# Performance work log

Measured on AMD Instinct MI355X. Metric: run time of the kernel, lower is better.

## Reference

```python
import jax, jax.numpy as jnp
import numpy as np

C = 256
DK = C // 8  # query/key channels


def setup_inputs() -> dict:
    key = jax.random.key(0)
    ks = jax.random.split(key, 7)
    B, W, H = 4, 64, 64
    x = jax.random.normal(ks[0], (B, C, W, H), dtype=jnp.float32)
    s_in = 1.0 / np.sqrt(C)
    Wq = jax.random.normal(ks[1], (DK, C), dtype=jnp.float32) * s_in
    bq = jnp.zeros((DK,), dtype=jnp.float32)
    Wk = jax.random.normal(ks[2], (DK, C), dtype=jnp.float32) * s_in
    bk = jnp.zeros((DK,), dtype=jnp.float32)
    Wv = jax.random.normal(ks[3], (C, C), dtype=jnp.float32) * s_in
    bv = jnp.zeros((C,), dtype=jnp.float32)
    return {"x": x, "Wq": Wq, "bq": bq, "Wk": Wk, "bk": bk, "Wv": Wv, "bv": bv}


def reference(x, Wq, bq, Wk, bk, Wv, bv):
    B, Cc, W, H = x.shape
    N = W * H
    xf = x.reshape(B, Cc, N)  # (B, C, N) flattened spatial
    # 1x1 convs == channel matmuls
    q = jnp.einsum('dc,bcn->bnd', Wq, xf) + bq  # (B, N, DK)
    k = jnp.einsum('dc,bcn->bdn', Wk, xf) + bk[None, :, None]  # (B, DK, N)
    v = jnp.einsum('oc,bcn->bon', Wv, xf) + bv[None, :, None]  # (B, C, N)
    energy = jnp.einsum('bnd,bdm->bnm', q, k) / jnp.sqrt(jnp.float32(q.shape[-1]))
    attn = jax.nn.softmax(energy, axis=-1)  # (B, N, N)
    out = jnp.einsum('bcn,bmn->bcm', v, attn)  # v @ attn^T
    return out.reshape(B, Cc, W, H) + x
```

## Files before the change

kernel.cpp:

```cpp
#include <hip/hip_runtime.h>
#include <hip/hip_bf16.h>
#include <math.h>

#define BB 4
#define CC 256
#define DKK 32
#define NN 4096
#define QSCALE2 0.25503489022324213f

typedef __attribute__((ext_vector_type(8))) __bf16 bf16x8;
typedef __attribute__((ext_vector_type(4))) __bf16 bf16x4;
typedef __attribute__((ext_vector_type(4))) float f32x4;

#define XROW 264

__global__ __launch_bounds__(256) void qkv2_kernel(
    const float* __restrict__ x,
    const float* __restrict__ Wq, const float* __restrict__ Wk,
    const float* __restrict__ Wv,
    const float* __restrict__ bq, const float* __restrict__ bk,
    const float* __restrict__ bv,
    __bf16* __restrict__ qws, __bf16* __restrict__ kws, __bf16* __restrict__ vws)
{
    __shared__ __align__(16) unsigned char smemB[32 * XROW * 2];
    __bf16* xs = (__bf16*)smemB;
    float (*scr)[33] = (float (*)[33])smemB;

    const int tid = threadIdx.x;
    const int w   = tid >> 6;
    const int l   = tid & 63;
    const int l15 = l & 15;
    const int lq  = l >> 4;
    const int n0  = blockIdx.x * 32;
    const int b   = blockIdx.y;

    {
        const int cl = tid >> 3;
        const int nf = (tid & 7) * 4;
#pragma unroll
        for (int p = 0; p < 8; p++) {
            int c = p * 32 + cl;
            float4 v = *(const float4*)&x[((size_t)(b * CC + c)) * NN + n0 + nf];
            xs[(nf + 0) * XROW + c] = (__bf16)v.x;
            xs[(nf + 1) * XROW + c] = (__bf16)v.y;
            xs[(nf + 2) * XROW + c] = (__bf16)v.z;
            xs[(nf + 3) * XROW + c] = (__bf16)v.w;
        }
    }

    const float* wrow[5];
#pragma unroll
    for (int ot = 0; ot < 5; ot++) {
        int ob = 80 * w + ot * 16;
        const float* mat; int r0;
        if (ob < 32)      { mat = Wq; r0 = ob; }
        else if (ob < 64) { mat = Wk; r0 = ob - 32; }
        else              { mat = Wv; r0 = ob - 64; }
        wrow[ot] = mat + (size_t)(r0 + l15) * CC + lq * 8;
    }

    __syncthreads();

    const f32x4 zf = {0.f, 0.f, 0.f, 0.f};
    f32x4 acc[5][2];
#pragma unroll
    for (int i = 0; i < 5; i++)
#pragma unroll
        for (int j = 0; j < 2; j++) acc[i][j] = zf;

    const __bf16* xls = &xs[l15 * XROW + lq * 8];

    bf16x8 bcur[2], acur[5], bnxt[2], anxt[5];
#pragma unroll
    for (int nt = 0; nt < 2; nt++) bcur[nt] = *(const bf16x8*)(xls + nt * 16 * XROW);
#pragma unroll
    for (int ot = 0; ot < 5; ot++) {
        f32x4 a0 = *(const f32x4*)(wrow[ot]);
        f32x4 a1 = *(const f32x4*)(wrow[ot] + 4);
        bf16x8 af;
#pragma unroll
        for (int j = 0; j < 4; j++) { af[j] = (__bf16)a0[j]; af[4 + j] = (__bf16)a1[j]; }
        acur[ot] = af;
    }

#pragma unroll
    for (int ks = 0; ks < 8; ks++) {
        if (ks < 7) {
#pragma unroll
            for (int nt = 0; nt < 2; nt++)
                bnxt[nt] = *(const bf16x8*)(xls + nt * 16 * XROW + (ks + 1) * 32);
#pragma unroll
            for (int ot = 0; ot < 5; ot++) {
                f32x4 a0 = *(const f32x4*)(wrow[ot] + (ks + 1) * 32);
                f32x4 a1 = *(const f32x4*)(wrow[ot] + (ks + 1) * 32 + 4);
                bf16x8 af;
#pragma unroll
                for (int j = 0; j < 4; j++) { af[j] = (__bf16)a0[j]; af[4 + j] = (__bf16)a1[j]; }
                anxt[ot] = af;
            }
        }
#pragma unroll
        for (int ot = 0; ot < 5; ot++)
#pragma unroll
            for (int nt = 0; nt < 2; nt++)
                acc[ot][nt] = __builtin_amdgcn_mfma_f32_16x16x32_bf16(acur[ot], bcur[nt], acc[ot][nt], 0, 0, 0);
        if (ks < 7) {
#pragma unroll
            for (int nt = 0; nt < 2; nt++) bcur[nt] = bnxt[nt];
#pragma unroll
            for (int ot = 0; ot < 5; ot++) acur[ot] = anxt[ot];
        }
    }

    __syncthreads();

    __bf16* vchunk = vws + (size_t)b * CC * NN + (size_t)(n0 >> 5) * 16 * 512;
#pragma unroll
    for (int ot = 0; ot < 5; ot++) {
        int ob = 80 * w + ot * 16;
#pragma unroll
        for (int nt = 0; nt < 2; nt++) {
#pragma unroll
            for (int r = 0; r < 4; r++) {
                int o = ob + lq * 4 + r;
                int n = nt * 16 + l15;
                float val = acc[ot][nt][r];
                if (ob >= 64) {
                    int c = o - 64;
                    vchunk[(5 * w - 4 + ot) * 512 + (lq * 4 + r) * 32 + n] =
                        (__bf16)(val + bv[c]);
                } else if (ob < 32) {
                    scr[o][n] = (val + bq[o]) * QSCALE2;
                } else {
                    scr[o][n] = val + bk[o - 32];
                }
            }
        }
    }
    __syncthreads();
    {
        int n  = tid >> 3;
        int d0 = (tid & 7) * 4;
        bf16x4 qv, kv;
#pragma unroll
        for (int j = 0; j < 4; j++) {
            qv[j] = (__bf16)scr[d0 + j][n];
            kv[j] = (__bf16)scr[32 + d0 + j][n];
        }
        size_t base = ((size_t)b * NN + n0 + n) * DKK + d0;
        *(bf16x4*)&qws[base] = qv;
        *(bf16x4*)&kws[base] = kv;
    }
}

#define PST 40
#define MST 68
#define PWSZ (64 * PST)

__global__ __launch_bounds__(256, 2) void attn_kernel(
    const __bf16* __restrict__ qb, const __bf16* __restrict__ kb,
    const __bf16* __restrict__ vt, const float* __restrict__ x,
    float* __restrict__ out)
{
    __shared__ __align__(16) unsigned char smem[42240];
    __bf16* pw   = (__bf16*)smem + (threadIdx.x >> 6) * 2 * PWSZ;
    float*  Ls   = (float*)(smem + 40960);
    float*  Linv = (float*)(smem + 41984);

    const int tid = threadIdx.x;
    const int w   = tid >> 6;
    const int l   = tid & 63;
    const int l15 = l & 15;
    const int lq  = l >> 4;

    const int beta = blockIdx.x;
    const int b    = (beta >> 1) & 3;
    const int ch   = (beta >> 3) & 1;
    const int mt   = ((beta >> 4) << 1) | (beta & 1);
    const int m0   = mt * 64;

    const __bf16* qbb = qb + (size_t)b * NN * DKK;
    const __bf16* kbb = kb + (size_t)b * NN * DKK;
    const __bf16* vtb = vt + (size_t)b * CC * NN;

    bf16x8 qa[4];
#pragma unroll
    for (int af = 0; af < 4; af++)
        qa[af] = *(const bf16x8*)(qbb + (size_t)(m0 + af * 16 + l15) * DKK + lq * 8);

    const __bf16* kstrip = kbb + (size_t)(w * 32 + l15) * DKK + lq * 8;
    const __bf16* vstrip = vtb + (size_t)w * 8192 + (size_t)ch * 4096
                               + l15 * 32 + lq * 8;

    const f32x4 zf = {0.f, 0.f, 0.f, 0.f};
    f32x4 acc[4][8];
#pragma unroll
    for (int i = 0; i < 4; i++)
#pragma unroll
        for (int j = 0; j < 8; j++) acc[i][j] = zf;
    float lacc[4] = {0.f, 0.f, 0.f, 0.f};

    bf16x8 kA0 = *(const bf16x8*)kstrip;
    bf16x8 kA1 = *(const bf16x8*)(kstrip + 16 * DKK);
#pragma unroll
    for (int af = 0; af < 4; af++) {
        f32x4 e0 = __builtin_amdgcn_mfma_f32_16x16x32_bf16(kA0, qa[af], zf, 0, 0, 0);
        f32x4 e1 = __builtin_amdgcn_mfma_f32_16x16x32_bf16(kA1, qa[af], zf, 0, 0, 0);
        bf16x4 p0, p1;
#pragma unroll
        for (int r = 0; r < 4; r++) {
            float v0 = __builtin_amdgcn_exp2f(e0[r]); lacc[af] += v0; p0[r] = (__bf16)v0;
            float v1 = __builtin_amdgcn_exp2f(e1[r]); lacc[af] += v1; p1[r] = (__bf16)v1;
        }
        *(bf16x4*)&pw[(af * 16 + l15) * PST + lq * 4]      = p0;
        *(bf16x4*)&pw[(af * 16 + l15) * PST + 16 + lq * 4] = p1;
    }
    kA0 = *(const bf16x8*)(kstrip + (size_t)128 * DKK);
    kA1 = *(const bf16x8*)(kstrip + (size_t)144 * DKK);

#pragma unroll 2
    for (int ic = 0; ic < 31; ic++) {
        const int cur = ic & 1;
        const __bf16* vch = vstrip + (size_t)ic * 32768;

        bf16x8 vfC[4], vfN[4];
#pragma unroll
        for (int ct = 0; ct < 4; ct++)
            vfC[ct] = *(const bf16x8*)(vch + ct * 512);

        bf16x8 pf[4];
#pragma unroll
        for (int af = 0; af < 4; af++)
            pf[af] = *(const bf16x8*)&pw[cur * PWSZ + (af * 16 + l15) * PST + lq * 8];

#pragma unroll
        for (int af = 0; af < 4; af++) {
            f32x4 e0 = __builtin_amdgcn_mfma_f32_16x16x32_bf16(kA0, qa[af], zf, 0, 0, 0);
            f32x4 e1 = __builtin_amdgcn_mfma_f32_16x16x32_bf16(kA1, qa[af], zf, 0, 0, 0);
            bf16x4 p0, p1;
#pragma unroll
            for (int r = 0; r < 4; r++) {
                float v0 = __builtin_amdgcn_exp2f(e0[r]); lacc[af] += v0; p0[r] = (__bf16)v0;
                float v1 = __builtin_amdgcn_exp2f(e1[r]); lacc[af] += v1; p1[r] = (__bf16)v1;
            }
            *(bf16x4*)&pw[(cur ^ 1) * PWSZ + (af * 16 + l15) * PST + lq * 4]      = p0;
            *(bf16x4*)&pw[(cur ^ 1) * PWSZ + (af * 16 + l15) * PST + 16 + lq * 4] = p1;
        }
        kA0 = *(const bf16x8*)(kstrip + (size_t)(ic + 2) * 128 * DKK);
        kA1 = *(const bf16x8*)(kstrip + (size_t)((ic + 2) * 128 + 16) * DKK);

#pragma unroll
        for (int ct = 0; ct < 4; ct++)
            vfN[ct] = *(const bf16x8*)(vch + (4 + ct) * 512);
        __builtin_amdgcn_s_setprio(1);
#pragma unroll
        for (int ct = 0; ct < 4; ct++)
#pragma unroll
            for (int af = 0; af < 4; af++)
                acc[af][ct] = __builtin_amdgcn_mfma_f32_16x16x32_bf16(vfC[ct], pf[af], acc[af][ct], 0, 0, 0);
#pragma unroll
        for (int ct = 0; ct < 4; ct++)
#pragma unroll
            for (int af = 0; af < 4; af++)
                acc[af][4 + ct] = __builtin_amdgcn_mfma_f32_16x16x32_bf16(vfN[ct], pf[af], acc[af][4 + ct], 0, 0, 0);
        __builtin_amdgcn_s_setprio(0);
    }

    {
        const __bf16* vch = vstrip + (size_t)31 * 32768;
        bf16x8 pf[4];
#pragma unroll
        for (int af = 0; af < 4; af++)
            pf[af] = *(const bf16x8*)&pw[(31 & 1) * PWSZ + (af * 16 + l15) * PST + lq * 8];
        bf16x8 vfC[4], vfN[4];
#pragma unroll
        for (int ct = 0; ct < 4; ct++) vfC[ct] = *(const bf16x8*)(vch + ct * 512);
#pragma unroll
        for (int ct = 0; ct < 4; ct++) vfN[ct] = *(const bf16x8*)(vch + (4 + ct) * 512);
        __builtin_amdgcn_s_setprio(1);
#pragma unroll
        for (int ct = 0; ct < 4; ct++)
#pragma unroll
            for (int af = 0; af < 4; af++)
                acc[af][ct] = __builtin_amdgcn_mfma_f32_16x16x32_bf16(vfC[ct], pf[af], acc[af][ct], 0, 0, 0);
#pragma unroll
        for (int ct = 0; ct < 4; ct++)
#pragma unroll
            for (int af = 0; af < 4; af++)
                acc[af][4 + ct] = __builtin_amdgcn_mfma_f32_16x16x32_bf16(vfN[ct], pf[af], acc[af][4 + ct], 0, 0, 0);
        __builtin_amdgcn_s_setprio(0);
    }

#pragma unroll
    for (int af = 0; af < 4; af++) {
        lacc[af] += __shfl_xor(lacc[af], 16, 64);
        lacc[af] += __shfl_xor(lacc[af], 32, 64);
    }
    if (lq == 0) {
#pragma unroll
        for (int af = 0; af < 4; af++) Ls[w * 64 + af * 16 + l15] = lacc[af];
    }
    __syncthreads();
    if (tid < 64)
        Linv[tid] = 1.0f / (Ls[tid] + Ls[64 + tid] + Ls[128 + tid] + Ls[192 + tid]);

    float* Ored = (float*)smem + w * (32 * MST);
#pragma unroll
    for (int q = 0; q < 4; q++) {
        if (q > 0) __syncthreads();
#pragma unroll
        for (int ctp = 0; ctp < 2; ctp++) {
            int ct = 2 * q + ctp;
#pragma unroll
            for (int af = 0; af < 4; af++) {
#pragma unroll
                for (int r = 0; r < 4; r++)
                    Ored[(ctp * 16 + lq * 4 + r) * MST + af * 16 + l15] = acc[af][ct][r];
            }
        }
        __syncthreads();
        const int cl  = tid >> 3;
        const int mi0 = (tid & 7) * 8;
        const float* Ob = (const float*)smem + cl * MST;
#pragma unroll
        for (int j = 0; j < 2; j++) {
            int mi = mi0 + 4 * j;
            f32x4 s = *(const f32x4*)&Ob[mi];
            s = s + *(const f32x4*)&Ob[1 * (32 * MST) + mi];
            s = s + *(const f32x4*)&Ob[2 * (32 * MST) + mi];
            s = s + *(const f32x4*)&Ob[3 * (32 * MST) + mi];
            f32x4 li = *(const f32x4*)&Linv[mi];
            int c = ch * 128 + q * 32 + cl;
            size_t gi = ((size_t)(b * CC + c)) * NN + m0 + mi;
            f32x4 xr = *(const f32x4*)&x[gi];
            *(f32x4*)&out[gi] = s * li + xr;
        }
    }
}

extern "C" void kernel_launch(void* const* d_in, const int* in_sizes, int n_in,
                              void* d_out, int out_size, void* d_ws, size_t ws_size,
                              hipStream_t stream) {
    const float* x  = (const float*)d_in[0];
    const float* Wq = (const float*)d_in[1];
    const float* bq = (const float*)d_in[2];
    const float* Wk = (const float*)d_in[3];
    const float* bk = (const float*)d_in[4];
    const float* Wv = (const float*)d_in[5];
    const float* bv = (const float*)d_in[6];
    float* out = (float*)d_out;

    __bf16* qws = (__bf16*)d_ws;
    __bf16* kws = qws + (size_t)BB * NN * DKK;
    __bf16* vws = kws + (size_t)BB * NN * DKK;

    qkv2_kernel<<<dim3(128, BB), 256, 0, stream>>>(x, Wq, Wk, Wv, bq, bk, bv,
                                                   qws, kws, vws);
    attn_kernel<<<dim3(512), 256, 0, stream>>>(qws, kws, vws, x, out);
}
```

Baseline: 149.3 us.

## Switch attention MFMAs to 32x32x16 tiles with swizzled P buffer and new V layout

```diff
diff --git a/kernel.cpp b/kernel.cpp
--- a/kernel.cpp
+++ b/kernel.cpp
@@ -11,6 +11,7 @@
 typedef __attribute__((ext_vector_type(8))) __bf16 bf16x8;
 typedef __attribute__((ext_vector_type(4))) __bf16 bf16x4;
 typedef __attribute__((ext_vector_type(4))) float f32x4;
+typedef __attribute__((ext_vector_type(16))) float f32x16;
 
 #define XROW 264
 
@@ -114,7 +115,7 @@
 
     __syncthreads();
 
-    __bf16* vchunk = vws + (size_t)b * CC * NN + (size_t)(n0 >> 5) * 16 * 512;
+    __bf16* vchunk = vws + (size_t)b * CC * NN + (size_t)(n0 >> 5) * 8192;
 #pragma unroll
     for (int ot = 0; ot < 5; ot++) {
         int ob = 80 * w + ot * 16;
@@ -126,8 +127,9 @@
                 int n = nt * 16 + l15;
                 float val = acc[ot][nt][r];
                 if (ob >= 64) {
-                    int c = o - 64;
-                    vchunk[(5 * w - 4 + ot) * 512 + (lq * 4 + r) * 32 + n] =
+                    int c  = o - 64;
+                    int ct = c >> 5, c5 = c & 31;
+                    vchunk[ct * 1024 + nt * 512 + c5 * 16 + l15] =
                         (__bf16)(val + bv[c]);
                 } else if (ob < 32) {
                     scr[o][n] = (val + bq[o]) * QSCALE2;
@@ -153,152 +155,156 @@
     }
 }
 
-#define PST 40
+#define PSTD 18
+#define PWB  (64 * PSTD * 4)
 #define MST 68
-#define PWSZ (64 * PST)
 
 __global__ __launch_bounds__(256, 2) void attn_kernel(
     const __bf16* __restrict__ qb, const __bf16* __restrict__ kb,
     const __bf16* __restrict__ vt, const float* __restrict__ x,
     float* __restrict__ out)
 {
-    __shared__ __align__(16) unsigned char smem[42240];
-    __bf16* pw   = (__bf16*)smem + (threadIdx.x >> 6) * 2 * PWSZ;
-    float*  Ls   = (float*)(smem + 40960);
-    float*  Linv = (float*)(smem + 41984);
-
+    __shared__ __align__(16) unsigned char smem[38144];
     const int tid = threadIdx.x;
     const int w   = tid >> 6;
     const int l   = tid & 63;
-    const int l15 = l & 15;
-    const int lq  = l >> 4;
+    const int m31 = l & 31;
+    const int hi  = l >> 5;
+    const int mx  = m31 & 3;
+    unsigned char* pwb = smem + w * 2 * PWB;
+    float* Ls   = (float*)(smem + 36864);
+    float* Linv = (float*)(smem + 37888);
 
     const int beta = blockIdx.x;
     const int b    = (beta >> 1) & 3;
     const int ch   = (beta >> 3) & 1;
-    const int mt   = ((beta >> 4) << 1) | (beta & 1);
-    const int m0   = mt * 64;
+    const int mt64 = ((beta >> 4) << 1) | (beta & 1);
+    const int m0   = mt64 * 64;
 
     const __bf16* qbb = qb + (size_t)b * NN * DKK;
     const __bf16* kbb = kb + (size_t)b * NN * DKK;
     const __bf16* vtb = vt + (size_t)b * CC * NN;
 
-    bf16x8 qa[4];
-#pragma unroll
-    for (int af = 0; af < 4; af++)
-        qa[af] = *(const bf16x8*)(qbb + (size_t)(m0 + af * 16 + l15) * DKK + lq * 8);
-
-    const __bf16* kstrip = kbb + (size_t)(w * 32 + l15) * DKK + lq * 8;
+    bf16x8 qa[2][2];
+#pragma unroll
+    for (int mt = 0; mt < 2; mt++)
+#pragma unroll
+        for (int kk = 0; kk < 2; kk++)
+            qa[mt][kk] = *(const bf16x8*)(qbb + (size_t)(m0 + mt * 32 + m31) * DKK + kk * 16 + hi * 8);
+
+    const __bf16* kstrip = kbb + (size_t)(w * 32 + m31) * DKK + hi * 8;
     const __bf16* vstrip = vtb + (size_t)w * 8192 + (size_t)ch * 4096
-                               + l15 * 32 + lq * 8;
-
-    const f32x4 zf = {0.f, 0.f, 0.f, 0.f};
-    f32x4 acc[4][8];
-#pragma unroll
-    for (int i = 0; i < 4; i++)
-#pragma unroll
-        for (int j = 0; j < 8; j++) acc[i][j] = zf;
-    float lacc[4] = {0.f, 0.f, 0.f, 0.f};
-
-    bf16x8 kA0 = *(const bf16x8*)kstrip;
-    bf16x8 kA1 = *(const bf16x8*)(kstrip + 16 * DKK);
-#pragma unroll
-    for (int af = 0; af < 4; af++) {
-        f32x4 e0 = __builtin_amdgcn_mfma_f32_16x16x32_bf16(kA0, qa[af], zf, 0, 0, 0);
-        f32x4 e1 = __builtin_amdgcn_mfma_f32_16x16x32_bf16(kA1, qa[af], zf, 0, 0, 0);
-        bf16x4 p0, p1;
-#pragma unroll
-        for (int r = 0; r < 4; r++) {
-            float v0 = __builtin_amdgcn_exp2f(e0[r]); lacc[af] += v0; p0[r] = (__bf16)v0;
-            float v1 = __builtin_amdgcn_exp2f(e1[r]); lacc[af] += v1; p1[r] = (__bf16)v1;
-        }
-        *(bf16x4*)&pw[(af * 16 + l15) * PST + lq * 4]      = p0;
-        *(bf16x4*)&pw[(af * 16 + l15) * PST + 16 + lq * 4] = p1;
-    }
-    kA0 = *(const bf16x8*)(kstrip + (size_t)128 * DKK);
-    kA1 = *(const bf16x8*)(kstrip + (size_t)144 * DKK);
+                               + m31 * 16 + hi * 8;
+
+    const f32x16 zf16 = {0.f,0.f,0.f,0.f,0.f,0.f,0.f,0.f,
+                         0.f,0.f,0.f,0.f,0.f,0.f,0.f,0.f};
+    f32x16 acc[4][2];
+#pragma unroll
+    for (int ct = 0; ct < 4; ct++)
+#pragma unroll
+        for (int mt = 0; mt < 2; mt++) acc[ct][mt] = zf16;
+    float lacc[2] = {0.f, 0.f};
+
+    auto kq_step = [&](int bufoff, bf16x8 kA0, bf16x8 kA1) {
+#pragma unroll
+        for (int mt = 0; mt < 2; mt++) {
+            f32x16 e = __builtin_amdgcn_mfma_f32_32x32x16_bf16(kA0, qa[mt][0], zf16, 0, 0, 0);
+            e = __builtin_amdgcn_mfma_f32_32x32x16_bf16(kA1, qa[mt][1], e, 0, 0, 0);
+            float s = 0.f;
+#pragma unroll
+            for (int g = 0; g < 4; g++) {
+                bf16x4 pb;
+#pragma unroll
+                for (int t = 0; t < 4; t++) {
+                    float v = __builtin_amdgcn_exp2f(e[4 * g + t]);
+                    s += v; pb[t] = (__bf16)v;
+                }
+                *(bf16x4*)(pwb + bufoff + (mt * 32 + m31) * 72 + ((g ^ mx) * 16 + hi * 8)) = pb;
+            }
+            lacc[mt] += s;
+        }
+    };
+
+    union PU { bf16x8 v; bf16x4 h[2]; };
+    auto pf_read = [&](int bufoff, bf16x8 (&pf)[2][2]) {
+#pragma unroll
+        for (int mt = 0; mt < 2; mt++)
+#pragma unroll
+            for (int kk = 0; kk < 2; kk++) {
+                int sb = (((kk * 2 + hi) ^ mx) * 16);
+                PU u;
+                u.h[0] = *(const bf16x4*)(pwb + bufoff + (mt * 32 + m31) * 72 + sb);
+                u.h[1] = *(const bf16x4*)(pwb + bufoff + (mt * 32 + m31) * 72 + sb + 8);
+                pf[mt][kk] = u.v;
+            }
+    };
+
+    {
+        bf16x8 kA0 = *(const bf16x8*)kstrip;
+        bf16x8 kA1 = *(const bf16x8*)(kstrip + 16);
+        kq_step(0, kA0, kA1);
+    }
+    bf16x8 kA0 = *(const bf16x8*)(kstrip + (size_t)128 * DKK);
+    bf16x8 kA1 = *(const bf16x8*)(kstrip + (size_t)128 * DKK + 16);
 
 #pragma unroll 2
     for (int ic = 0; ic < 31; ic++) {
         const int cur = ic & 1;
         const __bf16* vch = vstrip + (size_t)ic * 32768;
 
-        bf16x8 vfC[4], vfN[4];
+        bf16x8 vA[4], vB[4];
 #pragma unroll
         for (int ct = 0; ct < 4; ct++)
-            vfC[ct] = *(const bf16x8*)(vch + ct * 512);
-
-        bf16x8 pf[4];
-#pragma unroll
-        for (int af = 0; af < 4; af++)
-            pf[af] = *(const bf16x8*)&pw[cur * PWSZ + (af * 16 + l15) * PST + lq * 8];
-
-#pragma unroll
-        for (int af = 0; af < 4; af++) {
-            f32x4 e0 = __builtin_amdgcn_mfma_f32_16x16x32_bf16(kA0, qa[af], zf, 0, 0, 0);
-            f32x4 e1 = __builtin_amdgcn_mfma_f32_16x16x32_bf16(kA1, qa[af], zf, 0, 0, 0);
-            bf16x4 p0, p1;
-#pragma unroll
-            for (int r = 0; r < 4; r++) {
-                float v0 = __builtin_amdgcn_exp2f(e0[r]); lacc[af] += v0; p0[r] = (__bf16)v0;
-                float v1 = __builtin_amdgcn_exp2f(e1[r]); lacc[af] += v1; p1[r] = (__bf16)v1;
-            }
-            *(bf16x4*)&pw[(cur ^ 1) * PWSZ + (af * 16 + l15) * PST + lq * 4]      = p0;
-            *(bf16x4*)&pw[(cur ^ 1) * PWSZ + (af * 16 + l15) * PST + 16 + lq * 4] = p1;
-        }
+            vA[ct] = *(const bf16x8*)(vch + ct * 1024);
+
+        bf16x8 pf[2][2];
+        pf_read(cur * PWB, pf);
+
+        kq_step((cur ^ 1) * PWB, kA0, kA1);
+
+#pragma unroll
+        for (int ct = 0; ct < 4; ct++)
+            vB[ct] = *(const bf16x8*)(vch + ct * 1024 + 512);
+
         kA0 = *(const bf16x8*)(kstrip + (size_t)(ic + 2) * 128 * DKK);
-        kA1 = *(const bf16x8*)(kstrip + (size_t)((ic + 2) * 128 + 16) * DKK);
-
+        kA1 = *(const bf16x8*)(kstrip + (size_t)(ic + 2) * 128 * DKK + 16);
+
+        __builtin_amdgcn_s_setprio(1);
 #pragma unroll
         for (int ct = 0; ct < 4; ct++)
-            vfN[ct] = *(const bf16x8*)(vch + (4 + ct) * 512);
-        __builtin_amdgcn_s_setprio(1);
-#pragma unroll
-        for (int ct = 0; ct < 4; ct++)
-#pragma unroll
-            for (int af = 0; af < 4; af++)
-                acc[af][ct] = __builtin_amdgcn_mfma_f32_16x16x32_bf16(vfC[ct], pf[af], acc[af][ct], 0, 0, 0);
-#pragma unroll
-        for (int ct = 0; ct < 4; ct++)
-#pragma unroll
-            for (int af = 0; af < 4; af++)
-                acc[af][4 + ct] = __builtin_amdgcn_mfma_f32_16x16x32_bf16(vfN[ct], pf[af], acc[af][4 + ct], 0, 0, 0);
+#pragma unroll
+            for (int mt = 0; mt < 2; mt++) {
+                acc[ct][mt] = __builtin_amdgcn_mfma_f32_32x32x16_bf16(vA[ct], pf[mt][0], acc[ct][mt], 0, 0, 0);
+                acc[ct][mt] = __builtin_amdgcn_mfma_f32_32x32x16_bf16(vB[ct], pf[mt][1], acc[ct][mt], 0, 0, 0);
+            }
         __builtin_amdgcn_s_setprio(0);
     }
 
     {
         const __bf16* vch = vstrip + (size_t)31 * 32768;
-        bf16x8 pf[4];
-#pragma unroll
-        for (int af = 0; af < 4; af++)
-            pf[af] = *(const bf16x8*)&pw[(31 & 1) * PWSZ + (af * 16 + l15) * PST + lq * 8];
-        bf16x8 vfC[4], vfN[4];
-#pragma unroll
-        for (int ct = 0; ct < 4; ct++) vfC[ct] = *(const bf16x8*)(vch + ct * 512);
-#pragma unroll
-        for (int ct = 0; ct < 4; ct++) vfN[ct] = *(const bf16x8*)(vch + (4 + ct) * 512);
+        bf16x8 pf[2][2];
+        pf_read(PWB, pf);
+        bf16x8 vA[4], vB[4];
+#pragma unroll
+        for (int ct = 0; ct < 4; ct++) vA[ct] = *(const bf16x8*)(vch + ct * 1024);
+#pragma unroll
+        for (int ct = 0; ct < 4; ct++) vB[ct] = *(const bf16x8*)(vch + ct * 1024 + 512);
         __builtin_amdgcn_s_setprio(1);
 #pragma unroll
         for (int ct = 0; ct < 4; ct++)
 #pragma unroll
-            for (int af = 0; af < 4; af++)
-                acc[af][ct] = __builtin_amdgcn_mfma_f32_16x16x32_bf16(vfC[ct], pf[af], acc[af][ct], 0, 0, 0);
-#pragma unroll
-        for (int ct = 0; ct < 4; ct++)
-#pragma unroll
-            for (int af = 0; af < 4; af++)
-                acc[af][4 + ct] = __builtin_amdgcn_mfma_f32_16x16x32_bf16(vfN[ct], pf[af], acc[af][4 + ct], 0, 0, 0);
+            for (int mt = 0; mt < 2; mt++) {
+                acc[ct][mt] = __builtin_amdgcn_mfma_f32_32x32x16_bf16(vA[ct], pf[mt][0], acc[ct][mt], 0, 0, 0);
+                acc[ct][mt] = __builtin_amdgcn_mfma_f32_32x32x16_bf16(vB[ct], pf[mt][1], acc[ct][mt], 0, 0, 0);
+            }
         __builtin_amdgcn_s_setprio(0);
     }
 
 #pragma unroll
-    for (int af = 0; af < 4; af++) {
-        lacc[af] += __shfl_xor(lacc[af], 16, 64);
-        lacc[af] += __shfl_xor(lacc[af], 32, 64);
-    }
-    if (lq == 0) {
-#pragma unroll
-        for (int af = 0; af < 4; af++) Ls[w * 64 + af * 16 + l15] = lacc[af];
+    for (int mt = 0; mt < 2; mt++) lacc[mt] += __shfl_xor(lacc[mt], 32, 64);
+    if (hi == 0) {
+#pragma unroll
+        for (int mt = 0; mt < 2; mt++) Ls[w * 64 + mt * 32 + m31] = lacc[mt];
     }
     __syncthreads();
     if (tid < 64)
@@ -309,15 +315,12 @@
     for (int q = 0; q < 4; q++) {
         if (q > 0) __syncthreads();
 #pragma unroll
-        for (int ctp = 0; ctp < 2; ctp++) {
-            int ct = 2 * q + ctp;
-#pragma unroll
-            for (int af = 0; af < 4; af++) {
-#pragma unroll
-                for (int r = 0; r < 4; r++)
-                    Ored[(ctp * 16 + lq * 4 + r) * MST + af * 16 + l15] = acc[af][ct][r];
-            }
-        }
+        for (int mt = 0; mt < 2; mt++)
+#pragma unroll
+            for (int reg = 0; reg < 16; reg++) {
+                int crow = (reg & 3) + 8 * (reg >> 2) + 4 * hi;
+                Ored[crow * MST + mt * 32 + m31] = acc[q][mt][reg];
+            }
         __syncthreads();
         const int cl  = tid >> 3;
         const int mi0 = (tid & 7) * 8;
```

New measurement: 150.8 us. Within noise of the previous version (+1.0%).
